# Kernel optimization log

Hardware: AMD Instinct MI355X
Metric: run time of the kernel (lower is better)

Reference implementation:

```python
import jax, jax.numpy as jnp
import numpy as np

N_NODES = 50000
N_EDGES = 800000
IN_CH = 128
HID = 64
HEADS = 4
OUT_CH = 64
NEG_SLOPE = 0.2
EPS = 1e-16


def setup_inputs() -> dict:
    key = jax.random.key(0)
    ks = jax.random.split(key, 12)
    x = jax.random.normal(ks[0], (N_NODES, IN_CH), dtype=jnp.float32)
    edge_index = jax.random.randint(ks[1], (2, N_EDGES), 0, N_NODES, dtype=jnp.int32)
    s1 = 1.0 / np.sqrt(IN_CH)
    s2 = 1.0 / np.sqrt(HID * HEADS)
    s3 = 1.0 / np.sqrt(HID)
    return {
        "x": x,
        "edge_index": edge_index,
        # conv1: in -> heads*hid, concat=True
        "W1": jax.random.normal(ks[2], (IN_CH, HEADS * HID), dtype=jnp.float32) * s1,
        "a_src1": jax.random.normal(ks[3], (HEADS, HID), dtype=jnp.float32) * s3,
        "a_dst1": jax.random.normal(ks[4], (HEADS, HID), dtype=jnp.float32) * s3,
        "b1": jnp.zeros((HEADS * HID,), dtype=jnp.float32),
        # conv2: heads*hid -> hid, heads=1
        "W2": jax.random.normal(ks[5], (HEADS * HID, HID), dtype=jnp.float32) * s2,
        "a_src2": jax.random.normal(ks[6], (1, HID), dtype=jnp.float32) * s3,
        "a_dst2": jax.random.normal(ks[7], (1, HID), dtype=jnp.float32) * s3,
        "b2": jnp.zeros((HID,), dtype=jnp.float32),
        # final linear hid -> out
        "Wl": jax.random.normal(ks[8], (HID, OUT_CH), dtype=jnp.float32) * s3,
        "bl": jnp.zeros((OUT_CH,), dtype=jnp.float32),
    }


def _gat_conv(x, src, dst, W, a_src, a_dst, b, heads, ch):
    # x: [N, F]; src/dst: [E'] (self loops already appended)
    N = x.shape[0]
    h = (x @ W).reshape(N, heads, ch)                      # [N, H, C]
    alpha_src = jnp.einsum('nhc,hc->nh', h, a_src)         # [N, H]
    alpha_dst = jnp.einsum('nhc,hc->nh', h, a_dst)         # [N, H]
    e = jax.nn.leaky_relu(alpha_src[src] + alpha_dst[dst], NEG_SLOPE)  # [E, H]
    # per-destination segment softmax (every node has a self loop -> no empty segments)
    e_max = jax.ops.segment_max(e, dst, num_segments=N)
    e = jnp.exp(e - e_max[dst])
    denom = jax.ops.segment_sum(e, dst, num_segments=N)
    alpha = e / (denom[dst] + EPS)                         # [E, H]
    msg = h[src] * alpha[:, :, None]                       # [E, H, C]
    out = jax.ops.segment_sum(msg, dst, num_segments=N)    # [N, H, C]
    return out.reshape(N, heads * ch) + b


def reference(x, edge_index, W1, a_src1, a_dst1, b1, W2, a_src2, a_dst2, b2, Wl, bl):
    N = x.shape[0]
    loops = jnp.arange(N, dtype=edge_index.dtype)
    src = jnp.concatenate([edge_index[0], loops])
    dst = jnp.concatenate([edge_index[1], loops])
    h = _gat_conv(x, src, dst, W1, a_src1, a_dst1, b1, HEADS, HID)
    h = jax.nn.relu(h)
    h = _gat_conv(h, src, dst, W2, a_src2, a_dst2, b2, 1, HID)
    return h @ Wl + bl
```

## Files before the change

### kernel.cpp

```cpp
#include <hip/hip_runtime.h>

#define N_NODES 50000
#define N_EDGES 800000
#define E_TOT   850000
#define IN_CH   128
#define HID     64
#define HEADS   4
#define C1      256
#define OUT_CH  64
#define NEG_SLOPE 0.2f
#define EPSV    1e-16f

typedef _Float16 half_t;
typedef _Float16 half2_t __attribute__((ext_vector_type(2)));
typedef _Float16 half8_t __attribute__((ext_vector_type(8)));
typedef float f32x4 __attribute__((ext_vector_type(4)));

__device__ __forceinline__ float lrelu(float v) {
    return (v > 0.f) ? v : NEG_SLOPE * v;
}

__device__ __forceinline__ void acc8(float (&a)[8], float w, float4 r) {
    half2_t p;
    p = __builtin_bit_cast(half2_t, r.x); a[0] = fmaf(w, (float)p[0], a[0]); a[1] = fmaf(w, (float)p[1], a[1]);
    p = __builtin_bit_cast(half2_t, r.y); a[2] = fmaf(w, (float)p[0], a[2]); a[3] = fmaf(w, (float)p[1], a[3]);
    p = __builtin_bit_cast(half2_t, r.z); a[4] = fmaf(w, (float)p[0], a[4]); a[5] = fmaf(w, (float)p[1], a[5]);
    p = __builtin_bit_cast(half2_t, r.w); a[6] = fmaf(w, (float)p[0], a[6]); a[7] = fmaf(w, (float)p[1], a[7]);
}

__global__ __launch_bounds__(256) void k_prep(const float* __restrict__ W1,
                                              const float* __restrict__ W2,
                                              half_t* __restrict__ W1T,
                                              half_t* __restrict__ W2T) {
    int i = blockIdx.x * 256 + threadIdx.x;
    if (i < IN_CH * C1) {
        int c = i >> 7, k = i & 127;
        W1T[i] = (half_t)W1[k * C1 + c];
    }
    int j = i - IN_CH * C1;
    if (j >= 0 && j < C1 * HID) {
        int c = j >> 8, k = j & 255;
        W2T[j] = (half_t)W2[k * HID + c];
    }
}

__global__ void k_count(const int* __restrict__ ei, int* __restrict__ deg) {
    int e = blockIdx.x * blockDim.x + threadIdx.x;
    if (e >= E_TOT) return;
    int d = (e < N_EDGES) ? ei[N_EDGES + e] : (e - N_EDGES);
    atomicAdd(&deg[d], 1);
}

#define SCAN_CH 1024
#define NB_SCAN ((N_NODES + SCAN_CH - 1) / SCAN_CH)

__global__ __launch_bounds__(256) void k_bsum(const int* __restrict__ deg,
                                              int* __restrict__ bsum) {
    const int b = blockIdx.x;
    const int tid = threadIdx.x;
    int sum = 0;
    for (int i = tid; i < SCAN_CH; i += 256) {
        int idx = b * SCAN_CH + i;
        sum += (idx < N_NODES) ? deg[idx] : 0;
    }
    #pragma unroll
    for (int d = 1; d < 64; d <<= 1) sum += __shfl_xor(sum, d, 64);
    __shared__ int ws[4];
    if ((tid & 63) == 0) ws[tid >> 6] = sum;
    __syncthreads();
    if (tid == 0) bsum[b] = ws[0] + ws[1] + ws[2] + ws[3];
}

__global__ void k_bscan(const int* __restrict__ bsum, int* __restrict__ boff,
                        int* __restrict__ rowptr) {
    int tid = threadIdx.x;
    int v = (tid < NB_SCAN) ? bsum[tid] : 0;
    int s = v;
    #pragma unroll
    for (int d = 1; d < 64; d <<= 1) {
        int t = __shfl_up(s, d, 64);
        if (tid >= d) s += t;
    }
    boff[tid] = s - v;
    if (tid == 0) rowptr[N_NODES] = E_TOT;
}

__global__ __launch_bounds__(1024) void k_scanf(const int* __restrict__ deg,
                                                const int* __restrict__ boff,
                                                int* __restrict__ rowptr,
                                                int* __restrict__ cursor) {
    const int b = blockIdx.x;
    const int tid = threadIdx.x;
    const int lane = tid & 63;
    const int wv = tid >> 6;
    const int i = b * SCAN_CH + tid;
    int v = (i < N_NODES) ? deg[i] : 0;
    int s = v;
    #pragma unroll
    for (int d = 1; d < 64; d <<= 1) {
        int t = __shfl_up(s, d, 64);
        if (lane >= d) s += t;
    }
    __shared__ int wsum[16];
    if (lane == 63) wsum[wv] = s;
    __syncthreads();
    if (wv == 0 && lane < 16) {
        int w = wsum[lane];
        #pragma unroll
        for (int d = 1; d < 16; d <<= 1) {
            int t = __shfl_up(w, d, 64);
            if (lane >= d) w += t;
        }
        wsum[lane] = w;
    }
    __syncthreads();
    int excl = boff[b] + ((wv > 0) ? wsum[wv - 1] : 0) + (s - v);
    if (i < N_NODES) { rowptr[i] = excl; cursor[i] = excl; }
}

__global__ void k_scatter(const int* __restrict__ ei, int* __restrict__ cursor,
                          int* __restrict__ csr_src) {
    int e = blockIdx.x * blockDim.x + threadIdx.x;
    if (e >= E_TOT) return;
    int s, d;
    if (e < N_EDGES) { s = ei[e]; d = ei[N_EDGES + e]; }
    else             { s = d = e - N_EDGES; }
    int pos = atomicAdd(&cursor[d], 1);
    csr_src[pos] = s;
}

#define XS1_LD 136
#define HS1_LD 264
__global__ __launch_bounds__(256) void k_gemm1(
    const float* __restrict__ x, const half_t* __restrict__ W1T,
    const float* __restrict__ a_s1, const float* __restrict__ a_d1,
    half_t* __restrict__ h1h, float* __restrict__ l1s, float* __restrict__ l1d) {
    __shared__ half_t xs[32 * XS1_LD];
    __shared__ half_t hs[32 * HS1_LD];
    const int base = blockIdx.x * 32;
    const int rows = min(32, N_NODES - base);
    const int tid = threadIdx.x;
    for (int idx = tid; idx < 32 * 16; idx += 256) {
        int row = idx >> 4, c8 = (idx & 15) * 8;
        half8_t hv = {0, 0, 0, 0, 0, 0, 0, 0};
        if (row < rows) {
            const float4 v0 = *(const float4*)(x + (size_t)(base + row) * IN_CH + c8);
            const float4 v1 = *(const float4*)(x + (size_t)(base + row) * IN_CH + c8 + 4);
            hv[0] = (half_t)v0.x; hv[1] = (half_t)v0.y; hv[2] = (half_t)v0.z; hv[3] = (half_t)v0.w;
            hv[4] = (half_t)v1.x; hv[5] = (half_t)v1.y; hv[6] = (half_t)v1.z; hv[7] = (half_t)v1.w;
        }
        *(half8_t*)(xs + row * XS1_LD + c8) = hv;
    }
    __syncthreads();
    const int lane = tid & 63;
    const int w = tid >> 6;
    const int cw = w * 64;
    const int lr = lane & 15;
    const int lg = lane >> 4;
    f32x4 acc[2][4];
    #pragma unroll
    for (int i = 0; i < 2; ++i)
        #pragma unroll
        for (int j = 0; j < 4; ++j)
            #pragma unroll
            for (int r = 0; r < 4; ++r) acc[i][j][r] = 0.f;

    #pragma unroll
    for (int kt = 0; kt < 4; ++kt) {
        const int k0 = kt * 32 + lg * 8;
        half8_t A0 = *(const half8_t*)(xs + lr * XS1_LD + k0);
        half8_t A1 = *(const half8_t*)(xs + (16 + lr) * XS1_LD + k0);
        #pragma unroll
        for (int ct = 0; ct < 4; ++ct) {
            half8_t B = *(const half8_t*)(W1T + (size_t)(cw + ct * 16 + lr) * IN_CH + k0);
            acc[0][ct] = __builtin_amdgcn_mfma_f32_16x16x32_f16(A0, B, acc[0][ct], 0, 0, 0);
            acc[1][ct] = __builtin_amdgcn_mfma_f32_16x16x32_f16(A1, B, acc[1][ct], 0, 0, 0);
        }
    }
    #pragma unroll
    for (int rt = 0; rt < 2; ++rt)
        #pragma unroll
        for (int ct = 0; ct < 4; ++ct)
            #pragma unroll
            for (int r = 0; r < 4; ++r)
                hs[(rt * 16 + lg * 4 + r) * HS1_LD + cw + ct * 16 + lr] = (half_t)acc[rt][ct][r];
    __syncthreads();
    for (int idx = tid; idx < 32 * 32; idx += 256) {
        int row = idx >> 5, c8 = (idx & 31) * 8;
        if (row < rows)
            *(float4*)(h1h + (size_t)(base + row) * C1 + c8) = *(const float4*)(hs + row * HS1_LD + c8);
    }
    {
        const int c4l = lane * 4;
        const float4 av = *(const float4*)(a_s1 + c4l);
        const float4 dv = *(const float4*)(a_d1 + c4l);
        #pragma unroll
        for (int i = 0; i < 8; ++i) {
            int row = w * 8 + i;
            if (row < rows) {
                float2 rr = *(const float2*)(hs + row * HS1_LD + c4l);
                half2_t ha = __builtin_bit_cast(half2_t, rr.x);
                half2_t hb = __builtin_bit_cast(half2_t, rr.y);
                float ps = (float)ha[0] * av.x + (float)ha[1] * av.y + (float)hb[0] * av.z + (float)hb[1] * av.w;
                float pd = (float)ha[0] * dv.x + (float)ha[1] * dv.y + (float)hb[0] * dv.z + (float)hb[1] * dv.w;
                #pragma unroll
                for (int d = 1; d < 16; d <<= 1) {
                    ps += __shfl_xor(ps, d, 64);
                    pd += __shfl_xor(pd, d, 64);
                }
                if ((lane & 15) == 0) {
                    int hh = lane >> 4;
                    l1s[(base + row) * HEADS + hh] = ps;
                    l1d[(base + row) * HEADS + hh] = pd;
                }
            }
        }
    }
}

__global__ __launch_bounds__(256) void k_agg1(
    const half_t* __restrict__ h1h, const float* __restrict__ l1s, const float* __restrict__ l1d,
    const int* __restrict__ rowptr, const int* __restrict__ csr_src,
    const float* __restrict__ b1, half_t* __restrict__ out1h) {
    const int tid = threadIdx.x;
    const int lane = tid & 63;
    const int wv = tid >> 6;
    const int n = blockIdx.x * 4 + wv;
    if (n >= N_NODES) return;
    const int beg = rowptr[n], end = rowptr[n + 1];
    const float4 ldv = *(const float4*)(l1d + (size_t)n * 4);
    const int half = lane >> 5;
    const int l32 = lane & 31;
    const int c8 = l32 * 8;
    const int hh = l32 >> 3;
    const float ldh = (hh & 2) ? ((hh & 1) ? ldv.w : ldv.z) : ((hh & 1) ? ldv.y : ldv.x);
    const float* l1sh = l1s + hh;
    const float4* hrows = (const float4*)h1h;
    float a[8] = {0.f, 0.f, 0.f, 0.f, 0.f, 0.f, 0.f, 0.f};
    float dn = 0.f;
    int e = beg + half;
    for (; e + 6 < end; e += 8) {
        int s0 = csr_src[e], s1 = csr_src[e + 2], s2 = csr_src[e + 4], s3 = csr_src[e + 6];
        float4 r0 = hrows[s0 * 32 + l32];
        float4 r1 = hrows[s1 * 32 + l32];
        float4 r2 = hrows[s2 * 32 + l32];
        float4 r3 = hrows[s3 * 32 + l32];
        float g0 = l1sh[s0 * 4] + ldh;
        float g1 = l1sh[s1 * 4] + ldh;
        float g2 = l1sh[s2 * 4] + ldh;
        float g3 = l1sh[s3 * 4] + ldh;
        float w0 = __expf(lrelu(g0));
        float w1 = __expf(lrelu(g1));
        float w2 = __expf(lrelu(g2));
        float w3 = __expf(lrelu(g3));
        dn += (w0 + w1) + (w2 + w3);
        acc8(a, w0, r0);
        acc8(a, w1, r1);
        acc8(a, w2, r2);
        acc8(a, w3, r3);
    }
    for (; e < end; e += 2) {
        int s0 = csr_src[e];
        float4 r0 = hrows[s0 * 32 + l32];
        float g0 = l1sh[s0 * 4] + ldh;
        float w0 = __expf(lrelu(g0));
        dn += w0;
        acc8(a, w0, r0);
    }
    #pragma unroll
    for (int j = 0; j < 8; ++j) a[j] += __shfl_xor(a[j], 32, 64);
    dn += __shfl_xor(dn, 32, 64);
    if (half == 0) {
        const float inv = 1.f / (dn + EPSV);
        const float4 bv0 = *(const float4*)(b1 + c8);
        const float4 bv1 = *(const float4*)(b1 + c8 + 4);
        half2_t p01, p23, p45, p67;
        p01[0] = (half_t)fmaxf(fmaf(a[0], inv, bv0.x), 0.f);
        p01[1] = (half_t)fmaxf(fmaf(a[1], inv, bv0.y), 0.f);
        p23[0] = (half_t)fmaxf(fmaf(a[2], inv, bv0.z), 0.f);
        p23[1] = (half_t)fmaxf(fmaf(a[3], inv, bv0.w), 0.f);
        p45[0] = (half_t)fmaxf(fmaf(a[4], inv, bv1.x), 0.f);
        p45[1] = (half_t)fmaxf(fmaf(a[5], inv, bv1.y), 0.f);
        p67[0] = (half_t)fmaxf(fmaf(a[6], inv, bv1.z), 0.f);
        p67[1] = (half_t)fmaxf(fmaf(a[7], inv, bv1.w), 0.f);
        float4 st;
        st.x = __builtin_bit_cast(float, p01);
        st.y = __builtin_bit_cast(float, p23);
        st.z = __builtin_bit_cast(float, p45);
        st.w = __builtin_bit_cast(float, p67);
        *(float4*)(out1h + (size_t)n * C1 + c8) = st;
    }
}

#define XS2_LD 264
#define HS2_LD 72
__global__ __launch_bounds__(256) void k_gemm2(
    const half_t* __restrict__ out1h, const half_t* __restrict__ W2T,
    const float* __restrict__ a_s2, const float* __restrict__ a_d2,
    half_t* __restrict__ h2h, float* __restrict__ l2s, float* __restrict__ l2d) {
    __shared__ half_t xs[32 * XS2_LD];
    __shared__ half_t hs[32 * HS2_LD];
    const int base = blockIdx.x * 32;
    const int rows = min(32, N_NODES - base);
    const int tid = threadIdx.x;
    for (int idx = tid; idx < 32 * 32; idx += 256) {
        int row = idx >> 5, c8 = (idx & 31) * 8;
        half8_t hv = {0, 0, 0, 0, 0, 0, 0, 0};
        if (row < rows) hv = *(const half8_t*)(out1h + (size_t)(base + row) * C1 + c8);
        *(half8_t*)(xs + row * XS2_LD + c8) = hv;
    }
    __syncthreads();
    const int lane = tid & 63;
    const int w = tid >> 6;
    const int lr = lane & 15;
    const int lg = lane >> 4;
    f32x4 acc0, acc1;
    #pragma unroll
    for (int r = 0; r < 4; ++r) { acc0[r] = 0.f; acc1[r] = 0.f; }
    #pragma unroll
    for (int kt = 0; kt < 8; ++kt) {
        const int k0 = kt * 32 + lg * 8;
        half8_t A0 = *(const half8_t*)(xs + lr * XS2_LD + k0);
        half8_t A1 = *(const half8_t*)(xs + (16 + lr) * XS2_LD + k0);
        half8_t B  = *(const half8_t*)(W2T + (size_t)(w * 16 + lr) * C1 + k0);
        acc0 = __builtin_amdgcn_mfma_f32_16x16x32_f16(A0, B, acc0, 0, 0, 0);
        acc1 = __builtin_amdgcn_mfma_f32_16x16x32_f16(A1, B, acc1, 0, 0, 0);
    }
    #pragma unroll
    for (int r = 0; r < 4; ++r) {
        hs[(lg * 4 + r) * HS2_LD + w * 16 + lr] = (half_t)acc0[r];
        hs[(16 + lg * 4 + r) * HS2_LD + w * 16 + lr] = (half_t)acc1[r];
    }
    __syncthreads();
    {
        int idx = tid;
        int row = idx >> 3, c8 = (idx & 7) * 8;
        if (row < rows)
            *(float4*)(h2h + (size_t)(base + row) * HID + c8) = *(const float4*)(hs + row * HS2_LD + c8);
    }
    {
        const float vas = a_s2[lane];
        const float vad = a_d2[lane];
        #pragma unroll
        for (int i = 0; i < 8; ++i) {
            int row = w * 8 + i;
            if (row < rows) {
                float v = (float)hs[row * HS2_LD + lane];
                float ps = v * vas, pd = v * vad;
                #pragma unroll
                for (int d = 1; d < 64; d <<= 1) {
                    ps += __shfl_xor(ps, d, 64);
                    pd += __shfl_xor(pd, d, 64);
                }
                if (lane == 0) { l2s[base + row] = ps; l2d[base + row] = pd; }
            }
        }
    }
}

__global__ __launch_bounds__(256) void k_agg2(
    const half_t* __restrict__ h2h, const float* __restrict__ l2s, const float* __restrict__ l2d,
    const int* __restrict__ rowptr, const int* __restrict__ csr_src,
    const float* __restrict__ b2, const float* __restrict__ Wl, const float* __restrict__ bl,
    float* __restrict__ out) {
    __shared__ float Wls[HID * OUT_CH];
    __shared__ float vsh[4][HID];
    const int tid = threadIdx.x;
    const int lane = tid & 63;
    const int wv = tid >> 6;
    for (int i = tid; i < HID * OUT_CH; i += 256) Wls[i] = Wl[i];
    const int n = blockIdx.x * 4 + wv;
    const bool active = (n < N_NODES);
    if (active) {
        const int beg = rowptr[n], end = rowptr[n + 1];
        const float ld = l2d[n];
        const int q = lane >> 4;
        const int l16 = lane & 15;
        const float2* h2rows = (const float2*)h2h;
        float a0 = 0.f, a1 = 0.f, a2 = 0.f, a3 = 0.f, dn = 0.f;
        int e = beg + q;
        for (; e + 12 < end; e += 16) {
            int s0 = csr_src[e], s1 = csr_src[e + 4], s2 = csr_src[e + 8], s3 = csr_src[e + 12];
            float2 v0 = h2rows[s0 * 16 + l16];
            float2 v1 = h2rows[s1 * 16 + l16];
            float2 v2 = h2rows[s2 * 16 + l16];
            float2 v3 = h2rows[s3 * 16 + l16];
            float g0 = l2s[s0] + ld;
            float g1 = l2s[s1] + ld;
            float g2 = l2s[s2] + ld;
            float g3 = l2s[s3] + ld;
            float w0 = __expf(lrelu(g0));
            float w1 = __expf(lrelu(g1));
            float w2 = __expf(lrelu(g2));
            float w3 = __expf(lrelu(g3));
            dn += (w0 + w1) + (w2 + w3);
            half2_t p;
            p = __builtin_bit_cast(half2_t, v0.x); a0 = fmaf(w0, (float)p[0], a0); a1 = fmaf(w0, (float)p[1], a1);
            p = __builtin_bit_cast(half2_t, v0.y); a2 = fmaf(w0, (float)p[0], a2); a3 = fmaf(w0, (float)p[1], a3);
            p = __builtin_bit_cast(half2_t, v1.x); a0 = fmaf(w1, (float)p[0], a0); a1 = fmaf(w1, (float)p[1], a1);
            p = __builtin_bit_cast(half2_t, v1.y); a2 = fmaf(w1, (float)p[0], a2); a3 = fmaf(w1, (float)p[1], a3);
            p = __builtin_bit_cast(half2_t, v2.x); a0 = fmaf(w2, (float)p[0], a0); a1 = fmaf(w2, (float)p[1], a1);
            p = __builtin_bit_cast(half2_t, v2.y); a2 = fmaf(w2, (float)p[0], a2); a3 = fmaf(w2, (float)p[1], a3);
            p = __builtin_bit_cast(half2_t, v3.x); a0 = fmaf(w3, (float)p[0], a0); a1 = fmaf(w3, (float)p[1], a1);
            p = __builtin_bit_cast(half2_t, v3.y); a2 = fmaf(w3, (float)p[0], a2); a3 = fmaf(w3, (float)p[1], a3);
        }
        for (; e < end; e += 4) {
            int s = csr_src[e];
            float2 v = h2rows[s * 16 + l16];
            float lg = l2s[s] + ld;
            float w = __expf(lrelu(lg));
            dn += w;
            half2_t p;
            p = __builtin_bit_cast(half2_t, v.x); a0 = fmaf(w, (float)p[0], a0); a1 = fmaf(w, (float)p[1], a1);
            p = __builtin_bit_cast(half2_t, v.y); a2 = fmaf(w, (float)p[0], a2); a3 = fmaf(w, (float)p[1], a3);
        }
        a0 += __shfl_xor(a0, 16, 64); a0 += __shfl_xor(a0, 32, 64);
        a1 += __shfl_xor(a1, 16, 64); a1 += __shfl_xor(a1, 32, 64);
        a2 += __shfl_xor(a2, 16, 64); a2 += __shfl_xor(a2, 32, 64);
        a3 += __shfl_xor(a3, 16, 64); a3 += __shfl_xor(a3, 32, 64);
        dn += __shfl_xor(dn, 16, 64); dn += __shfl_xor(dn, 32, 64);
        if (q == 0) {
            const float inv = 1.f / (dn + EPSV);
            const float4 bv = *(const float4*)(b2 + l16 * 4);
            float4 vv;
            vv.x = fmaf(a0, inv, bv.x);
            vv.y = fmaf(a1, inv, bv.y);
            vv.z = fmaf(a2, inv, bv.z);
            vv.w = fmaf(a3, inv, bv.w);
            *(float4*)(&vsh[wv][l16 * 4]) = vv;
        }
    }
    __syncthreads();
    if (active) {
        float o = bl[lane];
        #pragma unroll
        for (int c2 = 0; c2 < HID; ++c2)
            o = fmaf(vsh[wv][c2], Wls[c2 * OUT_CH + lane], o);
        out[(size_t)n * OUT_CH + lane] = o;
    }
}

extern "C" void kernel_launch(void* const* d_in, const int* in_sizes, int n_in,
                              void* d_out, int out_size, void* d_ws, size_t ws_size,
                              hipStream_t stream) {
    const float* x   = (const float*)d_in[0];
    const int*   ei  = (const int*)d_in[1];
    const float* W1  = (const float*)d_in[2];
    const float* as1 = (const float*)d_in[3];
    const float* ad1 = (const float*)d_in[4];
    const float* b1  = (const float*)d_in[5];
    const float* W2  = (const float*)d_in[6];
    const float* as2 = (const float*)d_in[7];
    const float* ad2 = (const float*)d_in[8];
    const float* b2  = (const float*)d_in[9];
    const float* Wl  = (const float*)d_in[10];
    const float* bl  = (const float*)d_in[11];
    float* out = (float*)d_out;

    char* p = (char*)d_ws;
    auto alloc = [&](size_t bytes) {
        char* r = p;
        p += (bytes + 255) & ~(size_t)255;
        return r;
    };
    int* deg      = (int*)alloc((size_t)N_NODES * 4);
    int* rowptr   = (int*)alloc((size_t)(N_NODES + 1) * 4);
    int* cursor   = (int*)alloc((size_t)N_NODES * 4);
    int* csr_src  = (int*)alloc((size_t)E_TOT * 4);
    int* bsum     = (int*)alloc(64 * 4);
    int* boff     = (int*)alloc(64 * 4);
    half_t* W1T   = (half_t*)alloc((size_t)IN_CH * C1 * 2);
    half_t* W2T   = (half_t*)alloc((size_t)C1 * HID * 2);
    half_t* h1h   = (half_t*)alloc((size_t)N_NODES * C1 * 2);
    float* l1s    = (float*)alloc((size_t)N_NODES * HEADS * 4);
    float* l1d    = (float*)alloc((size_t)N_NODES * HEADS * 4);
    half_t* out1h = (half_t*)alloc((size_t)N_NODES * C1 * 2);
    half_t* h2h   = (half_t*)alloc((size_t)N_NODES * HID * 2);
    float* l2s    = (float*)alloc((size_t)N_NODES * 4);
    float* l2d    = (float*)alloc((size_t)N_NODES * 4);

    (void)hipMemsetAsync(deg, 0, (size_t)N_NODES * 4, stream);
    k_prep<<<(IN_CH * C1 + C1 * HID + 255) / 256, 256, 0, stream>>>(W1, W2, W1T, W2T);
    k_count<<<(E_TOT + 255) / 256, 256, 0, stream>>>(ei, deg);
    k_bsum<<<NB_SCAN, 256, 0, stream>>>(deg, bsum);
    k_bscan<<<1, 64, 0, stream>>>(bsum, boff, rowptr);
    k_scanf<<<NB_SCAN, 1024, 0, stream>>>(deg, boff, rowptr, cursor);
    k_scatter<<<(E_TOT + 255) / 256, 256, 0, stream>>>(ei, cursor, csr_src);
    k_gemm1<<<(N_NODES + 31) / 32, 256, 0, stream>>>(x, W1T, as1, ad1, h1h, l1s, l1d);
    k_agg1<<<(N_NODES + 3) / 4, 256, 0, stream>>>(h1h, l1s, l1d, rowptr, csr_src, b1, out1h);
    k_gemm2<<<(N_NODES + 31) / 32, 256, 0, stream>>>(out1h, W2T, as2, ad2, h2h, l2s, l2d);
    k_agg2<<<(N_NODES + 3) / 4, 256, 0, stream>>>(h2h, l2s, l2d, rowptr, csr_src, b2, Wl, bl, out);
}
```

Measured before the change: 264.9 us.

## Fuse layer-1 aggregation into GEMM2 and merge small prep/scan launches

```diff
diff --git a/kernel.cpp b/kernel.cpp
--- a/kernel.cpp
+++ b/kernel.cpp
@@ -28,27 +28,32 @@
     p = __builtin_bit_cast(half2_t, r.w); a[6] = fmaf(w, (float)p[0], a[6]); a[7] = fmaf(w, (float)p[1], a[7]);
 }
 
-__global__ __launch_bounds__(256) void k_prep(const float* __restrict__ W1,
-                                              const float* __restrict__ W2,
-                                              half_t* __restrict__ W1T,
-                                              half_t* __restrict__ W2T) {
-    int i = blockIdx.x * 256 + threadIdx.x;
-    if (i < IN_CH * C1) {
-        int c = i >> 7, k = i & 127;
-        W1T[i] = (half_t)W1[k * C1 + c];
-    }
-    int j = i - IN_CH * C1;
-    if (j >= 0 && j < C1 * HID) {
-        int c = j >> 8, k = j & 255;
-        W2T[j] = (half_t)W2[k * HID + c];
-    }
-}
-
-__global__ void k_count(const int* __restrict__ ei, int* __restrict__ deg) {
-    int e = blockIdx.x * blockDim.x + threadIdx.x;
-    if (e >= E_TOT) return;
-    int d = (e < N_EDGES) ? ei[N_EDGES + e] : (e - N_EDGES);
-    atomicAdd(&deg[d], 1);
+#define NPREP ((IN_CH * C1 + C1 * HID + 255) / 256)
+#define NCNT  ((E_TOT + 255) / 256)
+__global__ __launch_bounds__(256) void k_count_prep(
+    const int* __restrict__ ei, int* __restrict__ deg,
+    const float* __restrict__ W1, const float* __restrict__ W2,
+    half_t* __restrict__ W1T, half_t* __restrict__ W2T) {
+    const int gb = blockIdx.x;
+    const int tid = threadIdx.x;
+    if (gb < NPREP) {
+        int i = gb * 256 + tid;
+        if (i < IN_CH * C1) {
+            int c = i >> 7, k = i & 127;
+            W1T[i] = (half_t)W1[k * C1 + c];
+        }
+        int j = i - IN_CH * C1;
+        if (j >= 0 && j < C1 * HID) {
+            int c = j >> 8, k = j & 255;
+            W2T[j] = (half_t)W2[k * HID + c];
+        }
+    } else {
+        int e = (gb - NPREP) * 256 + tid;
+        if (e < E_TOT) {
+            int d = (e < N_EDGES) ? ei[N_EDGES + e] : (e - N_EDGES);
+            atomicAdd(&deg[d], 1);
+        }
+    }
 }
 
 #define SCAN_CH 1024
@@ -71,28 +76,23 @@
     if (tid == 0) bsum[b] = ws[0] + ws[1] + ws[2] + ws[3];
 }
 
-__global__ void k_bscan(const int* __restrict__ bsum, int* __restrict__ boff,
-                        int* __restrict__ rowptr) {
-    int tid = threadIdx.x;
-    int v = (tid < NB_SCAN) ? bsum[tid] : 0;
-    int s = v;
-    #pragma unroll
-    for (int d = 1; d < 64; d <<= 1) {
-        int t = __shfl_up(s, d, 64);
-        if (tid >= d) s += t;
-    }
-    boff[tid] = s - v;
-    if (tid == 0) rowptr[N_NODES] = E_TOT;
-}
-
 __global__ __launch_bounds__(1024) void k_scanf(const int* __restrict__ deg,
-                                                const int* __restrict__ boff,
+                                                const int* __restrict__ bsum,
                                                 int* __restrict__ rowptr,
                                                 int* __restrict__ cursor) {
+    __shared__ int wsum[16];
+    __shared__ int boff_s;
     const int b = blockIdx.x;
     const int tid = threadIdx.x;
     const int lane = tid & 63;
     const int wv = tid >> 6;
+    if (wv == 0) {
+        int v = (lane < b) ? bsum[lane] : 0;
+        #pragma unroll
+        for (int d = 1; d < 64; d <<= 1) v += __shfl_xor(v, d, 64);
+        if (lane == 0) boff_s = v;
+    }
+    if (b == 0 && tid == 0) rowptr[N_NODES] = E_TOT;
     const int i = b * SCAN_CH + tid;
     int v = (i < N_NODES) ? deg[i] : 0;
     int s = v;
@@ -101,7 +101,6 @@
         int t = __shfl_up(s, d, 64);
         if (lane >= d) s += t;
     }
-    __shared__ int wsum[16];
     if (lane == 63) wsum[wv] = s;
     __syncthreads();
     if (wv == 0 && lane < 16) {
@@ -114,7 +113,7 @@
         wsum[lane] = w;
     }
     __syncthreads();
-    int excl = boff[b] + ((wv > 0) ? wsum[wv - 1] : 0) + (s - v);
+    int excl = boff_s + ((wv > 0) ? wsum[wv - 1] : 0) + (s - v);
     if (i < N_NODES) { rowptr[i] = excl; cursor[i] = excl; }
 }
 
@@ -218,84 +217,12 @@
     }
 }
 
-__global__ __launch_bounds__(256) void k_agg1(
+#define XS2_LD 264
+#define HS2_LD 72
+__global__ __launch_bounds__(256) void k_agg1g2(
     const half_t* __restrict__ h1h, const float* __restrict__ l1s, const float* __restrict__ l1d,
     const int* __restrict__ rowptr, const int* __restrict__ csr_src,
-    const float* __restrict__ b1, half_t* __restrict__ out1h) {
-    const int tid = threadIdx.x;
-    const int lane = tid & 63;
-    const int wv = tid >> 6;
-    const int n = blockIdx.x * 4 + wv;
-    if (n >= N_NODES) return;
-    const int beg = rowptr[n], end = rowptr[n + 1];
-    const float4 ldv = *(const float4*)(l1d + (size_t)n * 4);
-    const int half = lane >> 5;
-    const int l32 = lane & 31;
-    const int c8 = l32 * 8;
-    const int hh = l32 >> 3;
-    const float ldh = (hh & 2) ? ((hh & 1) ? ldv.w : ldv.z) : ((hh & 1) ? ldv.y : ldv.x);
-    const float* l1sh = l1s + hh;
-    const float4* hrows = (const float4*)h1h;
-    float a[8] = {0.f, 0.f, 0.f, 0.f, 0.f, 0.f, 0.f, 0.f};
-    float dn = 0.f;
-    int e = beg + half;
-    for (; e + 6 < end; e += 8) {
-        int s0 = csr_src[e], s1 = csr_src[e + 2], s2 = csr_src[e + 4], s3 = csr_src[e + 6];
-        float4 r0 = hrows[s0 * 32 + l32];
-        float4 r1 = hrows[s1 * 32 + l32];
-        float4 r2 = hrows[s2 * 32 + l32];
-        float4 r3 = hrows[s3 * 32 + l32];
-        float g0 = l1sh[s0 * 4] + ldh;
-        float g1 = l1sh[s1 * 4] + ldh;
-        float g2 = l1sh[s2 * 4] + ldh;
-        float g3 = l1sh[s3 * 4] + ldh;
-        float w0 = __expf(lrelu(g0));
-        float w1 = __expf(lrelu(g1));
-        float w2 = __expf(lrelu(g2));
-        float w3 = __expf(lrelu(g3));
-        dn += (w0 + w1) + (w2 + w3);
-        acc8(a, w0, r0);
-        acc8(a, w1, r1);
-        acc8(a, w2, r2);
-        acc8(a, w3, r3);
-    }
-    for (; e < end; e += 2) {
-        int s0 = csr_src[e];
-        float4 r0 = hrows[s0 * 32 + l32];
-        float g0 = l1sh[s0 * 4] + ldh;
-        float w0 = __expf(lrelu(g0));
-        dn += w0;
-        acc8(a, w0, r0);
-    }
-    #pragma unroll
-    for (int j = 0; j < 8; ++j) a[j] += __shfl_xor(a[j], 32, 64);
-    dn += __shfl_xor(dn, 32, 64);
-    if (half == 0) {
-        const float inv = 1.f / (dn + EPSV);
-        const float4 bv0 = *(const float4*)(b1 + c8);
-        const float4 bv1 = *(const float4*)(b1 + c8 + 4);
-        half2_t p01, p23, p45, p67;
-        p01[0] = (half_t)fmaxf(fmaf(a[0], inv, bv0.x), 0.f);
-        p01[1] = (half_t)fmaxf(fmaf(a[1], inv, bv0.y), 0.f);
-        p23[0] = (half_t)fmaxf(fmaf(a[2], inv, bv0.z), 0.f);
-        p23[1] = (half_t)fmaxf(fmaf(a[3], inv, bv0.w), 0.f);
-        p45[0] = (half_t)fmaxf(fmaf(a[4], inv, bv1.x), 0.f);
-        p45[1] = (half_t)fmaxf(fmaf(a[5], inv, bv1.y), 0.f);
-        p67[0] = (half_t)fmaxf(fmaf(a[6], inv, bv1.z), 0.f);
-        p67[1] = (half_t)fmaxf(fmaf(a[7], inv, bv1.w), 0.f);
-        float4 st;
-        st.x = __builtin_bit_cast(float, p01);
-        st.y = __builtin_bit_cast(float, p23);
-        st.z = __builtin_bit_cast(float, p45);
-        st.w = __builtin_bit_cast(float, p67);
-        *(float4*)(out1h + (size_t)n * C1 + c8) = st;
-    }
-}
-
-#define XS2_LD 264
-#define HS2_LD 72
-__global__ __launch_bounds__(256) void k_gemm2(
-    const half_t* __restrict__ out1h, const half_t* __restrict__ W2T,
+    const float* __restrict__ b1, const half_t* __restrict__ W2T,
     const float* __restrict__ a_s2, const float* __restrict__ a_d2,
     half_t* __restrict__ h2h, float* __restrict__ l2s, float* __restrict__ l2d) {
     __shared__ half_t xs[32 * XS2_LD];
@@ -303,15 +230,72 @@
     const int base = blockIdx.x * 32;
     const int rows = min(32, N_NODES - base);
     const int tid = threadIdx.x;
-    for (int idx = tid; idx < 32 * 32; idx += 256) {
-        int row = idx >> 5, c8 = (idx & 31) * 8;
-        half8_t hv = {0, 0, 0, 0, 0, 0, 0, 0};
-        if (row < rows) hv = *(const half8_t*)(out1h + (size_t)(base + row) * C1 + c8);
-        *(half8_t*)(xs + row * XS2_LD + c8) = hv;
-    }
-    __syncthreads();
     const int lane = tid & 63;
-    const int w = tid >> 6;
+    const int wv = tid >> 6;
+    const int half = lane >> 5;
+    const int l32 = lane & 31;
+    const int c8 = l32 * 8;
+    const int hh = l32 >> 3;
+    const float* l1sh = l1s + hh;
+    const float4* hrows = (const float4*)h1h;
+    for (int i = 0; i < 8; ++i) {
+        const int row = wv * 8 + i;
+        const int n = base + row;
+        half8_t pk = {0, 0, 0, 0, 0, 0, 0, 0};
+        if (n < N_NODES) {
+            const int beg = rowptr[n], end = rowptr[n + 1];
+            const float4 ldv = *(const float4*)(l1d + (size_t)n * 4);
+            const float ldh = (hh & 2) ? ((hh & 1) ? ldv.w : ldv.z) : ((hh & 1) ? ldv.y : ldv.x);
+            float a[8] = {0.f, 0.f, 0.f, 0.f, 0.f, 0.f, 0.f, 0.f};
+            float dn = 0.f;
+            int e = beg + half;
+            for (; e + 6 < end; e += 8) {
+                int s0 = csr_src[e], s1 = csr_src[e + 2], s2 = csr_src[e + 4], s3 = csr_src[e + 6];
+                float4 r0 = hrows[s0 * 32 + l32];
+                float4 r1 = hrows[s1 * 32 + l32];
+                float4 r2 = hrows[s2 * 32 + l32];
+                float4 r3 = hrows[s3 * 32 + l32];
+                float g0 = l1sh[s0 * 4] + ldh;
+                float g1 = l1sh[s1 * 4] + ldh;
+                float g2 = l1sh[s2 * 4] + ldh;
+                float g3 = l1sh[s3 * 4] + ldh;
+                float w0 = __expf(lrelu(g0));
+                float w1 = __expf(lrelu(g1));
+                float w2 = __expf(lrelu(g2));
+                float w3 = __expf(lrelu(g3));
+                dn += (w0 + w1) + (w2 + w3);
+                acc8(a, w0, r0);
+                acc8(a, w1, r1);
+                acc8(a, w2, r2);
+                acc8(a, w3, r3);
+            }
+            for (; e < end; e += 2) {
+                int s0 = csr_src[e];
+                float4 r0 = hrows[s0 * 32 + l32];
+                float g0 = l1sh[s0 * 4] + ldh;
+                float w0 = __expf(lrelu(g0));
+                dn += w0;
+                acc8(a, w0, r0);
+            }
+            #pragma unroll
+            for (int j = 0; j < 8; ++j) a[j] += __shfl_xor(a[j], 32, 64);
+            dn += __shfl_xor(dn, 32, 64);
+            const float inv = 1.f / (dn + EPSV);
+            const float4 bv0 = *(const float4*)(b1 + c8);
+            const float4 bv1 = *(const float4*)(b1 + c8 + 4);
+            pk[0] = (half_t)fmaxf(fmaf(a[0], inv, bv0.x), 0.f);
+            pk[1] = (half_t)fmaxf(fmaf(a[1], inv, bv0.y), 0.f);
+            pk[2] = (half_t)fmaxf(fmaf(a[2], inv, bv0.z), 0.f);
+            pk[3] = (half_t)fmaxf(fmaf(a[3], inv, bv0.w), 0.f);
+            pk[4] = (half_t)fmaxf(fmaf(a[4], inv, bv1.x), 0.f);
+            pk[5] = (half_t)fmaxf(fmaf(a[5], inv, bv1.y), 0.f);
+            pk[6] = (half_t)fmaxf(fmaf(a[6], inv, bv1.z), 0.f);
+            pk[7] = (half_t)fmaxf(fmaf(a[7], inv, bv1.w), 0.f);
+        }
+        if (half == 0) *(half8_t*)(xs + row * XS2_LD + c8) = pk;
+    }
+    __syncthreads();
+    const int w = wv;
     const int lr = lane & 15;
     const int lg = lane >> 4;
     f32x4 acc0, acc1;
@@ -334,9 +318,9 @@
     __syncthreads();
     {
         int idx = tid;
-        int row = idx >> 3, c8 = (idx & 7) * 8;
+        int row = idx >> 3, cc8 = (idx & 7) * 8;
         if (row < rows)
-            *(float4*)(h2h + (size_t)(base + row) * HID + c8) = *(const float4*)(hs + row * HS2_LD + c8);
+            *(float4*)(h2h + (size_t)(base + row) * HID + cc8) = *(const float4*)(hs + row * HS2_LD + cc8);
     }
     {
         const float vas = a_s2[lane];
@@ -468,26 +452,22 @@
     int* cursor   = (int*)alloc((size_t)N_NODES * 4);
     int* csr_src  = (int*)alloc((size_t)E_TOT * 4);
     int* bsum     = (int*)alloc(64 * 4);
-    int* boff     = (int*)alloc(64 * 4);
     half_t* W1T   = (half_t*)alloc((size_t)IN_CH * C1 * 2);
     half_t* W2T   = (half_t*)alloc((size_t)C1 * HID * 2);
     half_t* h1h   = (half_t*)alloc((size_t)N_NODES * C1 * 2);
     float* l1s    = (float*)alloc((size_t)N_NODES * HEADS * 4);
     float* l1d    = (float*)alloc((size_t)N_NODES * HEADS * 4);
-    half_t* out1h = (half_t*)alloc((size_t)N_NODES * C1 * 2);
     half_t* h2h   = (half_t*)alloc((size_t)N_NODES * HID * 2);
     float* l2s    = (float*)alloc((size_t)N_NODES * 4);
     float* l2d    = (float*)alloc((size_t)N_NODES * 4);
 
     (void)hipMemsetAsync(deg, 0, (size_t)N_NODES * 4, stream);
-    k_prep<<<(IN_CH * C1 + C1 * HID + 255) / 256, 256, 0, stream>>>(W1, W2, W1T, W2T);
-    k_count<<<(E_TOT + 255) / 256, 256, 0, stream>>>(ei, deg);
+    k_count_prep<<<NPREP + NCNT, 256, 0, stream>>>(ei, deg, W1, W2, W1T, W2T);
     k_bsum<<<NB_SCAN, 256, 0, stream>>>(deg, bsum);
-    k_bscan<<<1, 64, 0, stream>>>(bsum, boff, rowptr);
-    k_scanf<<<NB_SCAN, 1024, 0, stream>>>(deg, boff, rowptr, cursor);
+    k_scanf<<<NB_SCAN, 1024, 0, stream>>>(deg, bsum, rowptr, cursor);
     k_scatter<<<(E_TOT + 255) / 256, 256, 0, stream>>>(ei, cursor, csr_src);
     k_gemm1<<<(N_NODES + 31) / 32, 256, 0, stream>>>(x, W1T, as1, ad1, h1h, l1s, l1d);
-    k_agg1<<<(N_NODES + 3) / 4, 256, 0, stream>>>(h1h, l1s, l1d, rowptr, csr_src, b1, out1h);
-    k_gemm2<<<(N_NODES + 31) / 32, 256, 0, stream>>>(out1h, W2T, as2, ad2, h2h, l2s, l2d);
+    k_agg1g2<<<(N_NODES + 31) / 32, 256, 0, stream>>>(h1h, l1s, l1d, rowptr, csr_src, b1,
+                                                      W2T, as2, ad2, h2h, l2s, l2d);
     k_agg2<<<(N_NODES + 3) / 4, 256, 0, stream>>>(h2h, l2s, l2d, rowptr, csr_src, b2, Wl, bl, out);
 }
```

Result: no change. 269.9 us (+1.9%).

## Merge independent setup kernels into shared launches to cut launch count

Applied to the files above, without the earlier changes.

```diff
diff --git a/kernel.cpp b/kernel.cpp
--- a/kernel.cpp
+++ b/kernel.cpp
@@ -28,27 +28,32 @@
     p = __builtin_bit_cast(half2_t, r.w); a[6] = fmaf(w, (float)p[0], a[6]); a[7] = fmaf(w, (float)p[1], a[7]);
 }
 
-__global__ __launch_bounds__(256) void k_prep(const float* __restrict__ W1,
-                                              const float* __restrict__ W2,
-                                              half_t* __restrict__ W1T,
-                                              half_t* __restrict__ W2T) {
-    int i = blockIdx.x * 256 + threadIdx.x;
-    if (i < IN_CH * C1) {
-        int c = i >> 7, k = i & 127;
-        W1T[i] = (half_t)W1[k * C1 + c];
-    }
-    int j = i - IN_CH * C1;
-    if (j >= 0 && j < C1 * HID) {
-        int c = j >> 8, k = j & 255;
-        W2T[j] = (half_t)W2[k * HID + c];
-    }
-}
-
-__global__ void k_count(const int* __restrict__ ei, int* __restrict__ deg) {
-    int e = blockIdx.x * blockDim.x + threadIdx.x;
-    if (e >= E_TOT) return;
-    int d = (e < N_EDGES) ? ei[N_EDGES + e] : (e - N_EDGES);
-    atomicAdd(&deg[d], 1);
+#define NPREP ((IN_CH * C1 + C1 * HID + 255) / 256)
+#define NCNT  ((E_TOT + 255) / 256)
+__global__ __launch_bounds__(256) void k_count_prep(
+    const int* __restrict__ ei, int* __restrict__ deg,
+    const float* __restrict__ W1, const float* __restrict__ W2,
+    half_t* __restrict__ W1T, half_t* __restrict__ W2T) {
+    const int gb = blockIdx.x;
+    const int tid = threadIdx.x;
+    if (gb < NPREP) {
+        int i = gb * 256 + tid;
+        if (i < IN_CH * C1) {
+            int c = i >> 7, k = i & 127;
+            W1T[i] = (half_t)W1[k * C1 + c];
+        }
+        int j = i - IN_CH * C1;
+        if (j >= 0 && j < C1 * HID) {
+            int c = j >> 8, k = j & 255;
+            W2T[j] = (half_t)W2[k * HID + c];
+        }
+    } else {
+        int e = (gb - NPREP) * 256 + tid;
+        if (e < E_TOT) {
+            int d = (e < N_EDGES) ? ei[N_EDGES + e] : (e - N_EDGES);
+            atomicAdd(&deg[d], 1);
+        }
+    }
 }
 
 #define SCAN_CH 1024
@@ -71,28 +76,23 @@
     if (tid == 0) bsum[b] = ws[0] + ws[1] + ws[2] + ws[3];
 }
 
-__global__ void k_bscan(const int* __restrict__ bsum, int* __restrict__ boff,
-                        int* __restrict__ rowptr) {
-    int tid = threadIdx.x;
-    int v = (tid < NB_SCAN) ? bsum[tid] : 0;
-    int s = v;
-    #pragma unroll
-    for (int d = 1; d < 64; d <<= 1) {
-        int t = __shfl_up(s, d, 64);
-        if (tid >= d) s += t;
-    }
-    boff[tid] = s - v;
-    if (tid == 0) rowptr[N_NODES] = E_TOT;
-}
-
 __global__ __launch_bounds__(1024) void k_scanf(const int* __restrict__ deg,
-                                                const int* __restrict__ boff,
+                                                const int* __restrict__ bsum,
                                                 int* __restrict__ rowptr,
                                                 int* __restrict__ cursor) {
+    __shared__ int wsum[16];
+    __shared__ int boff_s;
     const int b = blockIdx.x;
     const int tid = threadIdx.x;
     const int lane = tid & 63;
     const int wv = tid >> 6;
+    if (wv == 0) {
+        int v = (lane < b) ? bsum[lane] : 0;
+        #pragma unroll
+        for (int d = 1; d < 64; d <<= 1) v += __shfl_xor(v, d, 64);
+        if (lane == 0) boff_s = v;
+    }
+    if (b == 0 && tid == 0) rowptr[N_NODES] = E_TOT;
     const int i = b * SCAN_CH + tid;
     int v = (i < N_NODES) ? deg[i] : 0;
     int s = v;
@@ -101,7 +101,6 @@
         int t = __shfl_up(s, d, 64);
         if (lane >= d) s += t;
     }
-    __shared__ int wsum[16];
     if (lane == 63) wsum[wv] = s;
     __syncthreads();
     if (wv == 0 && lane < 16) {
@@ -114,32 +113,35 @@
         wsum[lane] = w;
     }
     __syncthreads();
-    int excl = boff[b] + ((wv > 0) ? wsum[wv - 1] : 0) + (s - v);
+    int excl = boff_s + ((wv > 0) ? wsum[wv - 1] : 0) + (s - v);
     if (i < N_NODES) { rowptr[i] = excl; cursor[i] = excl; }
 }
 
-__global__ void k_scatter(const int* __restrict__ ei, int* __restrict__ cursor,
-                          int* __restrict__ csr_src) {
-    int e = blockIdx.x * blockDim.x + threadIdx.x;
-    if (e >= E_TOT) return;
-    int s, d;
-    if (e < N_EDGES) { s = ei[e]; d = ei[N_EDGES + e]; }
-    else             { s = d = e - N_EDGES; }
-    int pos = atomicAdd(&cursor[d], 1);
-    csr_src[pos] = s;
-}
-
+#define NSCAT ((E_TOT + 255) / 256)
+#define NG1   ((N_NODES + 31) / 32)
 #define XS1_LD 136
 #define HS1_LD 264
-__global__ __launch_bounds__(256) void k_gemm1(
+__global__ __launch_bounds__(256) void k_scat_g1(
+    const int* __restrict__ ei, int* __restrict__ cursor, int* __restrict__ csr_src,
     const float* __restrict__ x, const half_t* __restrict__ W1T,
     const float* __restrict__ a_s1, const float* __restrict__ a_d1,
     half_t* __restrict__ h1h, float* __restrict__ l1s, float* __restrict__ l1d) {
     __shared__ half_t xs[32 * XS1_LD];
     __shared__ half_t hs[32 * HS1_LD];
-    const int base = blockIdx.x * 32;
+    const int tid = threadIdx.x;
+    if (blockIdx.x < NSCAT) {
+        int e = blockIdx.x * 256 + tid;
+        if (e < E_TOT) {
+            int s, d;
+            if (e < N_EDGES) { s = ei[e]; d = ei[N_EDGES + e]; }
+            else             { s = d = e - N_EDGES; }
+            int pos = atomicAdd(&cursor[d], 1);
+            csr_src[pos] = s;
+        }
+        return;
+    }
+    const int base = (blockIdx.x - NSCAT) * 32;
     const int rows = min(32, N_NODES - base);
-    const int tid = threadIdx.x;
     for (int idx = tid; idx < 32 * 16; idx += 256) {
         int row = idx >> 4, c8 = (idx & 15) * 8;
         half8_t hv = {0, 0, 0, 0, 0, 0, 0, 0};
@@ -468,7 +470,6 @@
     int* cursor   = (int*)alloc((size_t)N_NODES * 4);
     int* csr_src  = (int*)alloc((size_t)E_TOT * 4);
     int* bsum     = (int*)alloc(64 * 4);
-    int* boff     = (int*)alloc(64 * 4);
     half_t* W1T   = (half_t*)alloc((size_t)IN_CH * C1 * 2);
     half_t* W2T   = (half_t*)alloc((size_t)C1 * HID * 2);
     half_t* h1h   = (half_t*)alloc((size_t)N_NODES * C1 * 2);
@@ -480,13 +481,11 @@
     float* l2d    = (float*)alloc((size_t)N_NODES * 4);
 
     (void)hipMemsetAsync(deg, 0, (size_t)N_NODES * 4, stream);
-    k_prep<<<(IN_CH * C1 + C1 * HID + 255) / 256, 256, 0, stream>>>(W1, W2, W1T, W2T);
-    k_count<<<(E_TOT + 255) / 256, 256, 0, stream>>>(ei, deg);
+    k_count_prep<<<NPREP + NCNT, 256, 0, stream>>>(ei, deg, W1, W2, W1T, W2T);
     k_bsum<<<NB_SCAN, 256, 0, stream>>>(deg, bsum);
-    k_bscan<<<1, 64, 0, stream>>>(bsum, boff, rowptr);
-    k_scanf<<<NB_SCAN, 1024, 0, stream>>>(deg, boff, rowptr, cursor);
-    k_scatter<<<(E_TOT + 255) / 256, 256, 0, stream>>>(ei, cursor, csr_src);
-    k_gemm1<<<(N_NODES + 31) / 32, 256, 0, stream>>>(x, W1T, as1, ad1, h1h, l1s, l1d);
+    k_scanf<<<NB_SCAN, 1024, 0, stream>>>(deg, bsum, rowptr, cursor);
+    k_scat_g1<<<NSCAT + NG1, 256, 0, stream>>>(ei, cursor, csr_src,
+                                               x, W1T, as1, ad1, h1h, l1s, l1d);
     k_agg1<<<(N_NODES + 3) / 4, 256, 0, stream>>>(h1h, l1s, l1d, rowptr, csr_src, b1, out1h);
     k_gemm2<<<(N_NODES + 31) / 32, 256, 0, stream>>>(out1h, W2T, as2, ad2, h2h, l2s, l2d);
     k_agg2<<<(N_NODES + 3) / 4, 256, 0, stream>>>(h2h, l2s, l2d, rowptr, csr_src, b2, Wl, bl, out);
```

After: 259.0 us. -2.3%, faster.
